# Kernel tuning notes

Hardware: AMD Instinct MI355X
Metric: run time of the kernel (lower is better)

The kernel has to match this reference:

```python
import jax, jax.numpy as jnp
import numpy as np
import math

N_HEAD, D_HEAD, D_MODEL = 12, 64, 768
ATT_SPAN = 512            # max_position_embeddings // stride**block_index
SCALE_FACTOR = 3          # 1 + 2 (relative attention: content + c2p + p2c)
CLS_TOKENS = 1            # num_highway_cls_tokens + 1
INF = 1e6
LN_EPS = 1e-5
SCALE = 1.0 / (math.sqrt(D_HEAD) * math.sqrt(SCALE_FACTOR))


def setup_inputs() -> dict:
    key = jax.random.key(0)
    ks = jax.random.split(key, 10)
    B, S = 2, 2048
    lin = lambda k, shape: jax.random.normal(k, shape, dtype=jnp.float32) * 0.02
    return {
        "query": jax.random.normal(ks[0], (B, S, D_MODEL), dtype=jnp.float32),
        "attention_mask": jnp.ones((B, S), dtype=jnp.float32),
        "pos_key_embed": jax.random.normal(ks[1], (2 * ATT_SPAN, D_MODEL), dtype=jnp.float32),
        "pos_query_embed": jax.random.normal(ks[2], (2 * ATT_SPAN, D_MODEL), dtype=jnp.float32),
        "Wq": lin(ks[3], (N_HEAD * D_HEAD, D_MODEL)),
        "bq": jnp.zeros((N_HEAD * D_HEAD,), dtype=jnp.float32),
        "Wk": lin(ks[4], (N_HEAD * D_HEAD, D_MODEL)),
        "Wv": lin(ks[5], (D_MODEL, D_MODEL)),
        "bv": jnp.zeros((D_MODEL,), dtype=jnp.float32),
        "Wpq": lin(ks[6], (N_HEAD * D_HEAD, D_MODEL)),
        "bpq": jnp.zeros((N_HEAD * D_HEAD,), dtype=jnp.float32),
        "Wpk": lin(ks[7], (N_HEAD * D_HEAD, D_MODEL)),
        "r_w_bias": jax.random.normal(ks[8], (N_HEAD, D_HEAD), dtype=jnp.float32) * 0.02,
        "ln_gamma": jnp.ones((D_MODEL,), dtype=jnp.float32),
        "ln_beta": jnp.zeros((D_MODEL,), dtype=jnp.float32),
    }


def _forward(query, attention_mask, pos_key_embed, pos_query_embed,
             Wq, bq, Wk, Wv, bv, Wpq, bpq, Wpk, r_w_bias, ln_gamma, ln_beta):
    B, S, _ = query.shape
    # self-attention: key = value = query
    v = query @ Wv.T + bv                                             # v_head projection
    qh = (query @ Wq.T + bq).reshape(B, S, N_HEAD, D_HEAD)
    kh = (query @ Wk.T).reshape(B, S, N_HEAD, D_HEAD)
    vh = v.reshape(B, S, N_HEAD, D_MODEL // N_HEAD)
    qh = (qh + r_w_bias) * SCALE                                       # bias + scale fused into q

    content = jnp.einsum('bind,bjnd->bnij', qh, kh)                    # [B,n,S,S]

    # ---- disentangled relative-position bias (DeBERTa-style c2p + p2c) ----
    pos_k = (pos_key_embed @ Wpk.T).reshape(2 * ATT_SPAN, N_HEAD, D_HEAD).transpose(1, 0, 2)          # [n,2span,d]
    pos_q = (pos_query_embed @ Wpq.T + bpq).reshape(2 * ATT_SPAN, N_HEAD, D_HEAD).transpose(1, 0, 2)  # [n,2span,d]
    qbn = qh.transpose(0, 2, 1, 3)                                     # [B,n,S,d] (already scaled)
    kbn = kh.transpose(0, 2, 1, 3)
    rel = jnp.arange(S)[:, None] - jnp.arange(S)[None, :]              # [S,S] query - key

    # content -> position
    c2p = jnp.einsum('bnid,njd->bnij', qbn, pos_k)                     # [B,n,S,2span]
    c2p_idx = jnp.clip(rel + ATT_SPAN, 0, 2 * ATT_SPAN - 1)
    c2p_score = jnp.take_along_axis(c2p, c2p_idx[None, None], axis=-1) # [B,n,S,S]

    # position -> content
    p2c = jnp.einsum('bnjd,nid->bnji', kbn * (1.0 / math.sqrt(D_HEAD * SCALE_FACTOR)), pos_q)  # [B,n,S,2span]
    p2c_idx = jnp.clip(-rel + ATT_SPAN, 0, 2 * ATT_SPAN - 1)
    p2c_score = jnp.take_along_axis(p2c, p2c_idx[None, None], axis=-1).swapaxes(-1, -2)        # [B,n,S,S]

    bias = c2p_score + p2c_score
    # zero out bias on cls rows and cls columns (the padding/concat trick in the source)
    keep = (jnp.arange(S) >= CLS_TOKENS).astype(bias.dtype)
    bias = bias * (keep[:, None] * keep[None, :])

    score = content + bias
    score = score - INF * (1.0 - attention_mask[:, None, None, :])
    prob = jax.nn.softmax(score, axis=-1)                              # attention_dropout = 0.0

    attn_vec = jnp.einsum('bnij,bjnd->bind', prob, vh).reshape(B, S, D_MODEL)
    # fused residual + LayerNorm(attn_out)
    mu = attn_vec.mean(-1, keepdims=True)
    var = ((attn_vec - mu) ** 2).mean(-1, keepdims=True)
    ln = (attn_vec - mu) / jnp.sqrt(var + LN_EPS) * ln_gamma + ln_beta
    return query + ln


def reference(query, attention_mask, pos_key_embed, pos_query_embed,
              Wq, bq, Wk, Wv, bv, Wpq, bpq, Wpk, r_w_bias, ln_gamma, ln_beta):
    return _forward(query, attention_mask, pos_key_embed, pos_query_embed,
                    Wq, bq, Wk, Wv, bv, Wpq, bpq, Wpk, r_w_bias, ln_gamma, ln_beta)
```

## Files before the change

### kernel.cpp

```cpp
#include <hip/hip_runtime.h>
#include <math.h>

#define NB     2
#define SEQ    2048
#define NHEAD  12
#define DMODEL 768
#define SPAN2  1024
#define SCALEF 0.07216878364870323f

typedef unsigned short ushort;
typedef unsigned int   uint;
typedef __attribute__((ext_vector_type(8))) short  bh8;
typedef __attribute__((ext_vector_type(4))) float  f32x4;
typedef __attribute__((ext_vector_type(4))) unsigned short us4;

__device__ inline ushort f2bf(float x) {
    uint u = __builtin_bit_cast(uint, x);
    u += 0x7FFFu + ((u >> 16) & 1u);
    return (ushort)(u >> 16);
}
__device__ inline float b2f(ushort h) {
    uint u = ((uint)h) << 16;
    return __builtin_bit_cast(float, u);
}

__device__ __forceinline__ void gld16(const ushort* g, ushort* l) {
    __builtin_amdgcn_global_load_lds(
        (const __attribute__((address_space(1))) void*)g,
        (__attribute__((address_space(3))) void*)l, 16, 0, 0);
}

__device__ __forceinline__ bh8 ldsfrag(const ushort* tile, int row, int slot) {
    return *(const bh8*)((const char*)tile + row * 128 + (((slot ^ (row & 7)) << 4)));
}

struct CvtArgs {
    const float* src[8];
    ushort*      dst[8];
    int          n[8];
};

__global__ __launch_bounds__(256) void cvt_bf16(CvtArgs a)
{
    const int seg = blockIdx.y;
    const int i   = (blockIdx.x * 256 + threadIdx.x) * 8;
    if (i >= a.n[seg]) return;
    const float4* s = (const float4*)(a.src[seg] + i);
    const float4 x = s[0], y = s[1];
    bh8 o;
    o[0] = (short)f2bf(x.x); o[1] = (short)f2bf(x.y);
    o[2] = (short)f2bf(x.z); o[3] = (short)f2bf(x.w);
    o[4] = (short)f2bf(y.x); o[5] = (short)f2bf(y.y);
    o[6] = (short)f2bf(y.z); o[7] = (short)f2bf(y.w);
    *(bh8*)(a.dst[seg] + i) = o;
}

__global__ __launch_bounds__(256) void proj_qkv(
    const ushort* __restrict__ X,
    const ushort* __restrict__ Wq, const ushort* __restrict__ Wk,
    const ushort* __restrict__ Wv,
    const float* __restrict__ bq, const float* __restrict__ rwb,
    const float* __restrict__ bv,
    ushort* __restrict__ qh, ushort* __restrict__ kh, ushort* __restrict__ vht)
{
    __shared__ ushort Xs [32 * 64];
    __shared__ ushort Wqs[64 * 64];
    __shared__ ushort Wks[64 * 64];
    __shared__ ushort Wvs[64 * 64];
    const int r0 = blockIdx.x * 32;
    const int n  = blockIdx.y;
    const int c0 = n * 64;
    const int tid  = threadIdx.x;
    const int w    = tid >> 6;
    const int lane = tid & 63;
    const int lo   = lane & 15;
    const int hi8  = (lane >> 4) * 8;
    const int g4   = (lane >> 4) * 4;
    const int wr   = w & 1;
    const int wc   = w >> 1;
    const int r8   = lane >> 3;
    const int sl   = lane & 7;
    const int slotA = hi8 >> 3;

    f32x4 aq[2] = {}, ak[2] = {}, av[2] = {};
    for (int k0 = 0; k0 < DMODEL; k0 += 64) {
        {
            const int r = w * 8 + r8;
            const int s = sl ^ (r & 7);
            gld16(X + (size_t)(r0 + r) * DMODEL + k0 + s * 8, Xs + w * 512);
        }
        #pragma unroll
        for (int i = 0; i < 2; ++i) {
            const int c = i * 4 + w;
            const int r = c * 8 + r8;
            const int s = sl ^ (r & 7);
            gld16(Wq + (size_t)(c0 + r) * DMODEL + k0 + s * 8, Wqs + c * 512);
            gld16(Wk + (size_t)(c0 + r) * DMODEL + k0 + s * 8, Wks + c * 512);
            gld16(Wv + (size_t)(c0 + r) * DMODEL + k0 + s * 8, Wvs + c * 512);
        }
        __syncthreads();
        const bh8 a0 = ldsfrag(Xs, wr * 16 + lo, slotA);
        const bh8 a1 = ldsfrag(Xs, wr * 16 + lo, 4 + slotA);
        #pragma unroll
        for (int ct = 0; ct < 2; ++ct) {
            const int row = wc * 32 + ct * 16 + lo;
            aq[ct] = __builtin_amdgcn_mfma_f32_16x16x32_bf16(a0, ldsfrag(Wqs, row, slotA),     aq[ct], 0, 0, 0);
            aq[ct] = __builtin_amdgcn_mfma_f32_16x16x32_bf16(a1, ldsfrag(Wqs, row, 4 + slotA), aq[ct], 0, 0, 0);
            ak[ct] = __builtin_amdgcn_mfma_f32_16x16x32_bf16(a0, ldsfrag(Wks, row, slotA),     ak[ct], 0, 0, 0);
            ak[ct] = __builtin_amdgcn_mfma_f32_16x16x32_bf16(a1, ldsfrag(Wks, row, 4 + slotA), ak[ct], 0, 0, 0);
            av[ct] = __builtin_amdgcn_mfma_f32_16x16x32_bf16(a0, ldsfrag(Wvs, row, slotA),     av[ct], 0, 0, 0);
            av[ct] = __builtin_amdgcn_mfma_f32_16x16x32_bf16(a1, ldsfrag(Wvs, row, 4 + slotA), av[ct], 0, 0, 0);
        }
        __syncthreads();
    }

    const int rbase = r0 + wr * 16 + g4;
    const int bb  = rbase >> 11;
    const int rr0 = rbase & (SEQ - 1);
    #pragma unroll
    for (int ct = 0; ct < 2; ++ct) {
        const int d = wc * 32 + ct * 16 + lo;
        const int c = c0 + d;
        const float bqv = bq[c] + rwb[c];
        const float bvv = bv[c];
        us4 o;
        #pragma unroll
        for (int reg = 0; reg < 4; ++reg) {
            const size_t rowi = ((size_t)bb * NHEAD + n) * SEQ + rr0 + reg;
            qh[rowi * 64 + d] = f2bf((aq[ct][reg] + bqv) * SCALEF);
            kh[rowi * 64 + d] = f2bf(ak[ct][reg]);
            o[reg] = f2bf(av[ct][reg] + bvv);
        }
        *(us4*)&vht[(((size_t)bb * NHEAD + n) * 64 + d) * SEQ + rr0] = o;
    }
}

__global__ __launch_bounds__(256) void proj_pos(
    const ushort* __restrict__ PKe, const ushort* __restrict__ PQe,
    const ushort* __restrict__ Wpk, const ushort* __restrict__ Wpq,
    const float* __restrict__ bpq,
    ushort* __restrict__ pkp, ushort* __restrict__ pqp)
{
    __shared__ ushort Xk [32 * 64];
    __shared__ ushort Xq [32 * 64];
    __shared__ ushort Wks[64 * 64];
    __shared__ ushort Wqs[64 * 64];
    const int r0 = blockIdx.x * 32;
    const int n  = blockIdx.y;
    const int c0 = n * 64;
    const int tid  = threadIdx.x;
    const int w    = tid >> 6;
    const int lane = tid & 63;
    const int lo   = lane & 15;
    const int hi8  = (lane >> 4) * 8;
    const int g4   = (lane >> 4) * 4;
    const int wr   = w & 1;
    const int wc   = w >> 1;
    const int r8   = lane >> 3;
    const int sl   = lane & 7;
    const int slotA = hi8 >> 3;

    f32x4 apk[2] = {}, apq[2] = {};
    for (int k0 = 0; k0 < DMODEL; k0 += 64) {
        {
            const int r = w * 8 + r8;
            const int s = sl ^ (r & 7);
            gld16(PKe + (size_t)(r0 + r) * DMODEL + k0 + s * 8, Xk + w * 512);
            gld16(PQe + (size_t)(r0 + r) * DMODEL + k0 + s * 8, Xq + w * 512);
        }
        #pragma unroll
        for (int i = 0; i < 2; ++i) {
            const int c = i * 4 + w;
            const int r = c * 8 + r8;
            const int s = sl ^ (r & 7);
            gld16(Wpk + (size_t)(c0 + r) * DMODEL + k0 + s * 8, Wks + c * 512);
            gld16(Wpq + (size_t)(c0 + r) * DMODEL + k0 + s * 8, Wqs + c * 512);
        }
        __syncthreads();
        const bh8 xk0 = ldsfrag(Xk, wr * 16 + lo, slotA);
        const bh8 xk1 = ldsfrag(Xk, wr * 16 + lo, 4 + slotA);
        const bh8 xq0 = ldsfrag(Xq, wr * 16 + lo, slotA);
        const bh8 xq1 = ldsfrag(Xq, wr * 16 + lo, 4 + slotA);
        #pragma unroll
        for (int ct = 0; ct < 2; ++ct) {
            const int row = wc * 32 + ct * 16 + lo;
            apk[ct] = __builtin_amdgcn_mfma_f32_16x16x32_bf16(xk0, ldsfrag(Wks, row, slotA),     apk[ct], 0, 0, 0);
            apk[ct] = __builtin_amdgcn_mfma_f32_16x16x32_bf16(xk1, ldsfrag(Wks, row, 4 + slotA), apk[ct], 0, 0, 0);
            apq[ct] = __builtin_amdgcn_mfma_f32_16x16x32_bf16(xq0, ldsfrag(Wqs, row, slotA),     apq[ct], 0, 0, 0);
            apq[ct] = __builtin_amdgcn_mfma_f32_16x16x32_bf16(xq1, ldsfrag(Wqs, row, 4 + slotA), apq[ct], 0, 0, 0);
        }
        __syncthreads();
    }

    const int rr0 = r0 + wr * 16 + g4;
    #pragma unroll
    for (int ct = 0; ct < 2; ++ct) {
        const int d = wc * 32 + ct * 16 + lo;
        const int c = c0 + d;
        const float badd = bpq[c];
        #pragma unroll
        for (int reg = 0; reg < 4; ++reg) {
            const size_t rowi = ((size_t)n * SPAN2 + rr0 + reg);
            pkp[rowi * 64 + d] = f2bf(apk[ct][reg]);
            pqp[rowi * 64 + d] = f2bf((apq[ct][reg] + badd) * SCALEF);
        }
    }
}

__global__ __launch_bounds__(256) void cd_vec(
    const ushort* __restrict__ qh, const ushort* __restrict__ kh,
    const ushort* __restrict__ posk, const ushort* __restrict__ posq,
    float* __restrict__ cdv)
{
    __shared__ float pr[4][64];
    const int bn = blockIdx.y;
    const int n  = bn % NHEAD;
    const int tid = threadIdx.x;
    if (tid < 64) {
        pr[0][tid] = b2f(posk[((size_t)n * SPAN2) * 64 + tid]);
        pr[1][tid] = b2f(posk[((size_t)n * SPAN2 + SPAN2 - 1) * 64 + tid]);
        pr[2][tid] = b2f(posq[((size_t)n * SPAN2) * 64 + tid]);
        pr[3][tid] = b2f(posq[((size_t)n * SPAN2 + SPAN2 - 1) * 64 + tid]);
    }
    __syncthreads();
    const int row = blockIdx.x * 32 + (tid >> 3);
    const int e0  = (tid & 7) * 8;
    const bh8 q8 = *(const bh8*)&qh[((size_t)bn * SEQ + row) * 64 + e0];
    const bh8 k8 = *(const bh8*)&kh[((size_t)bn * SEQ + row) * 64 + e0];
    float a0 = 0.f, a1 = 0.f, a2 = 0.f, a3 = 0.f;
    #pragma unroll
    for (int t = 0; t < 8; ++t) {
        const float qv = b2f((ushort)q8[t]);
        const float kv = b2f((ushort)k8[t]);
        a0 += qv * pr[0][e0 + t];
        a1 += qv * pr[1][e0 + t];
        a2 += kv * pr[2][e0 + t];
        a3 += kv * pr[3][e0 + t];
    }
    #pragma unroll
    for (int off = 1; off <= 4; off <<= 1) {
        a0 += __shfl_xor(a0, off);
        a1 += __shfl_xor(a1, off);
        a2 += __shfl_xor(a2, off);
        a3 += __shfl_xor(a3, off);
    }
    if ((tid & 7) == 0) {
        cdv[((size_t)0 * NB * NHEAD + bn) * SEQ + row] = a0;
        cdv[((size_t)1 * NB * NHEAD + bn) * SEQ + row] = a1;
        cdv[((size_t)2 * NB * NHEAD + bn) * SEQ + row] = a2;
        cdv[((size_t)3 * NB * NHEAD + bn) * SEQ + row] = a3;
    }
}

__global__ __launch_bounds__(256, 3) void attn_mfma10(
    const ushort* __restrict__ qh, const ushort* __restrict__ kh,
    const ushort* __restrict__ vht, const ushort* __restrict__ posk,
    const ushort* __restrict__ posq, const float* __restrict__ mask,
    const float* __restrict__ cdv, float* __restrict__ attn)
{
    __shared__ ushort POS[128 * 64];
    __shared__ ushort Kb [64 * 64];
    __shared__ ushort Vb [64 * 64];
    __shared__ ushort T1c[64 * 68];
    __shared__ ushort T2c[64 * 68];

    const int id   = blockIdx.x;
    const int xcd  = id & 7;
    const int slot = id >> 3;
    const int bn   = xcd * 3 + (slot >> 5);
    const int i0   = (slot & 31) * 64;
    const int b    = bn / NHEAD;
    const int n    = bn % NHEAD;

    const int tid  = threadIdx.x;
    const int w    = tid >> 6;
    const int lane = tid & 63;
    const int lo   = lane & 15;
    const int hi8  = (lane >> 4) * 8;
    const int g4   = (lane >> 4) * 4;
    const int w16  = w * 16;
    const int r8   = lane >> 3;
    const int sl   = lane & 7;
    const int slotA = hi8 >> 3;

    const ushort* qrow = qh + ((size_t)bn * SEQ + i0 + w16 + lo) * 64;
    const bh8 qa0 = *(const bh8*)&qrow[hi8];
    const bh8 qa1 = *(const bh8*)&qrow[32 + hi8];

    const ushort* khb = kh   + (size_t)bn * SEQ * 64;
    const ushort* vtb = vht  + (size_t)bn * 64 * SEQ;
    const ushort* pkh = posk + (size_t)n * SPAN2 * 64;
    const ushort* pqh = posq + (size_t)n * SPAN2 * 64;
    const float*  mrw = mask + (size_t)b * SEQ;

    float C0r[4], C1r[4];
    {
        const float* C0p = cdv + (size_t)bn * SEQ;
        const float* C1p = cdv + ((size_t)NB * NHEAD + bn) * SEQ;
        #pragma unroll
        for (int reg = 0; reg < 4; ++reg) {
            C0r[reg] = C0p[i0 + w16 + g4 + reg];
            C1r[reg] = C1p[i0 + w16 + g4 + reg];
        }
    }
    const float* D0p = cdv + ((size_t)2 * NB * NHEAD + bn) * SEQ;
    const float* D1p = cdv + ((size_t)3 * NB * NHEAD + bn) * SEQ;

    f32x4 accPV[4] = {};
    float mrow[4] = {-1e30f, -1e30f, -1e30f, -1e30f};
    float lrow[4] = {0.f, 0.f, 0.f, 0.f};

    for (int j0 = 0; j0 < SEQ; j0 += 64) {
        const int d0base = i0 - j0 + 449;
        const bool clamp0 = (d0base <= -126);
        const bool clamp1 = (d0base >= 1023);

        if (!clamp0 && !clamp1) {
        #pragma unroll
        for (int i = 0; i < 2; ++i) {
            const int c = i * 4 + w;
            const int r = c * 8 + r8;
            const int s = sl ^ (r & 7);
            gld16(khb + (size_t)(j0 + r) * 64 + s * 8, Kb + c * 512);
        }
        #pragma unroll
        for (int i = 0; i < 4; ++i) {
            const int c = i * 4 + w;
            const int r = c * 8 + r8;
            const int s = sl ^ (r & 7);
            int gr = d0base + r; gr = gr < 0 ? 0 : (gr > SPAN2 - 1 ? SPAN2 - 1 : gr);
            gld16(pkh + (size_t)gr * 64 + s * 8, POS + c * 512);
        }
        __syncthreads();

        const bh8 ka0 = ldsfrag(Kb, w16 + lo, slotA);
        const bh8 ka1 = ldsfrag(Kb, w16 + lo, 4 + slotA);
        f32x4 z1[5];
        #pragma unroll
        for (int q = 0; q < 5; ++q) {
            const int u1 = (w + q) * 16 + lo;
            const bh8 pk0 = ldsfrag(POS, u1, slotA);
            const bh8 pk1 = ldsfrag(POS, u1, 4 + slotA);
            f32x4 a = {};
            a = __builtin_amdgcn_mfma_f32_16x16x32_bf16(qa0, pk0, a, 0, 0, 0);
            z1[q] = __builtin_amdgcn_mfma_f32_16x16x32_bf16(qa1, pk1, a, 0, 0, 0);
        }
        __syncthreads();

        #pragma unroll
        for (int i = 0; i < 4; ++i) {
            const int c = i * 4 + w;
            const int r = c * 8 + r8;
            const int s = sl ^ (r & 7);
            int gr = d0base + r; gr = gr < 0 ? 0 : (gr > SPAN2 - 1 ? SPAN2 - 1 : gr);
            gld16(pqh + (size_t)gr * 64 + s * 8, POS + c * 512);
        }
        #pragma unroll
        for (int i = 0; i < 2; ++i) {
            const int c = i * 4 + w;
            const int r = c * 8 + r8;
            const int s = sl ^ (r & 7);
            gld16(vtb + (size_t)r * SEQ + j0 + s * 8, Vb + c * 512);
        }
        #pragma unroll
        for (int q = 0; q < 5; ++q)
            #pragma unroll
            for (int reg = 0; reg < 4; ++reg) {
                const int cc2 = q * 16 + lo - g4 - reg;
                if (cc2 >= 0 && cc2 < 64)
                    T1c[(w16 + g4 + reg) * 68 + cc2] = f2bf(z1[q][reg]);
            }
        f32x4 accS[4];
        #pragma unroll
        for (int ct = 0; ct < 4; ++ct) {
            const bh8 kb0 = ldsfrag(Kb, ct * 16 + lo, slotA);
            const bh8 kb1 = ldsfrag(Kb, ct * 16 + lo, 4 + slotA);
            f32x4 z = {};
            z = __builtin_amdgcn_mfma_f32_16x16x32_bf16(qa0, kb0, z, 0, 0, 0);
            accS[ct] = __builtin_amdgcn_mfma_f32_16x16x32_bf16(qa1, kb1, z, 0, 0, 0);
        }
        float maskadd[4];
        #pragma unroll
        for (int ct = 0; ct < 4; ++ct)
            maskadd[ct] = -1e6f * (1.f - mrw[j0 + ct * 16 + lo]);
        __syncthreads();

        #pragma unroll
        for (int q = 0; q < 5; ++q) {
            const int u2 = (3 - w + q) * 16 + lo;
            const bh8 pq0 = ldsfrag(POS, u2, slotA);
            const bh8 pq1 = ldsfrag(POS, u2, 4 + slotA);
            f32x4 z = {};
            z = __builtin_amdgcn_mfma_f32_16x16x32_bf16(ka0, pq0, z, 0, 0, 0);
            z = __builtin_amdgcn_mfma_f32_16x16x32_bf16(ka1, pq1, z, 0, 0, 0);
            #pragma unroll
            for (int reg = 0; reg < 4; ++reg) {
                const int il2 = q * 16 + lo + g4 + reg - 15;
                if (il2 >= 0 && il2 < 64)
                    T2c[(w16 + g4 + reg) * 68 + il2] = f2bf(z[reg]);
            }
        }
        __syncthreads();

        float corr[4];
        char* pbase = (char*)POS + w * 2048;
        #pragma unroll
        for (int reg = 0; reg < 4; ++reg) {
            const int il = w16 + g4 + reg;
            const int gi = i0 + il;
            float s[4], rmax = -1e30f;
            #pragma unroll
            for (int ct = 0; ct < 4; ++ct) {
                const int jl = ct * 16 + lo;
                float v = accS[ct][reg];
                if (gi >= 1 && (j0 + jl) >= 1)
                    v += b2f(T1c[il * 68 + 63 - jl]) + b2f(T2c[jl * 68 + il]);
                v += maskadd[ct];
                s[ct] = v;
                rmax = fmaxf(rmax, v);
            }
            rmax = fmaxf(rmax, __shfl_xor(rmax, 1));
            rmax = fmaxf(rmax, __shfl_xor(rmax, 2));
            rmax = fmaxf(rmax, __shfl_xor(rmax, 4));
            rmax = fmaxf(rmax, __shfl_xor(rmax, 8));
            const float mnew = fmaxf(mrow[reg], rmax);
            const float cc   = __expf(mrow[reg] - mnew);
            float psum = 0.f;
            const int prow = g4 + reg;
            #pragma unroll
            for (int ct = 0; ct < 4; ++ct) {
                const float p = __expf(s[ct] - mnew);
                psum += p;
                *(ushort*)(pbase + prow * 128 + ((((ct * 16 + lo) * 2)) ^ ((prow & 7) * 16))) = f2bf(p);
            }
            psum += __shfl_xor(psum, 1);
            psum += __shfl_xor(psum, 2);
            psum += __shfl_xor(psum, 4);
            psum += __shfl_xor(psum, 8);
            lrow[reg] = lrow[reg] * cc + psum;
            mrow[reg] = mnew;
            corr[reg] = cc;
        }

        {
            const bh8 pa0 = *(const bh8*)(pbase + lo * 128 + ((slotA << 4) ^ ((lo & 7) * 16)));
            const bh8 pa1 = *(const bh8*)(pbase + lo * 128 + (((4 + slotA) << 4) ^ ((lo & 7) * 16)));
            #pragma unroll
            for (int dt = 0; dt < 4; ++dt) {
                const bh8 vb0 = ldsfrag(Vb, dt * 16 + lo, slotA);
                const bh8 vb1 = ldsfrag(Vb, dt * 16 + lo, 4 + slotA);
                f32x4 a = accPV[dt];
                #pragma unroll
                for (int reg = 0; reg < 4; ++reg) a[reg] *= corr[reg];
                a = __builtin_amdgcn_mfma_f32_16x16x32_bf16(pa0, vb0, a, 0, 0, 0);
                accPV[dt] = __builtin_amdgcn_mfma_f32_16x16x32_bf16(pa1, vb1, a, 0, 0, 0);
            }
        }
        __syncthreads();

        } else {
        const float* Dp = clamp0 ? D0p : D1p;
        float Dvv[4];
        #pragma unroll
        for (int ct = 0; ct < 4; ++ct)
            Dvv[ct] = Dp[j0 + ct * 16 + lo];
        float maskadd[4];
        #pragma unroll
        for (int ct = 0; ct < 4; ++ct)
            maskadd[ct] = -1e6f * (1.f - mrw[j0 + ct * 16 + lo]);

        #pragma unroll
        for (int i = 0; i < 2; ++i) {
            const int c = i * 4 + w;
            const int r = c * 8 + r8;
            const int s = sl ^ (r & 7);
            gld16(khb + (size_t)(j0 + r) * 64 + s * 8, Kb + c * 512);
            gld16(vtb + (size_t)r * SEQ + j0 + s * 8, Vb + c * 512);
        }
        __syncthreads();

        f32x4 accS[4];
        #pragma unroll
        for (int ct = 0; ct < 4; ++ct) {
            const bh8 kb0 = ldsfrag(Kb, ct * 16 + lo, slotA);
            const bh8 kb1 = ldsfrag(Kb, ct * 16 + lo, 4 + slotA);
            f32x4 z = {};
            z = __builtin_amdgcn_mfma_f32_16x16x32_bf16(qa0, kb0, z, 0, 0, 0);
            accS[ct] = __builtin_amdgcn_mfma_f32_16x16x32_bf16(qa1, kb1, z, 0, 0, 0);
        }

        float corr[4];
        char* pbase = (char*)POS + w * 2048;
        #pragma unroll
        for (int reg = 0; reg < 4; ++reg) {
            const int il = w16 + g4 + reg;
            const int gi = i0 + il;
            const float Cvv = clamp0 ? C0r[reg] : C1r[reg];
            float s[4], rmax = -1e30f;
            #pragma unroll
            for (int ct = 0; ct < 4; ++ct) {
                const int jl = ct * 16 + lo;
                float v = accS[ct][reg];
                if (gi >= 1 && (j0 + jl) >= 1)
                    v += Cvv + Dvv[ct];
                v += maskadd[ct];
                s[ct] = v;
                rmax = fmaxf(rmax, v);
            }
            rmax = fmaxf(rmax, __shfl_xor(rmax, 1));
            rmax = fmaxf(rmax, __shfl_xor(rmax, 2));
            rmax = fmaxf(rmax, __shfl_xor(rmax, 4));
            rmax = fmaxf(rmax, __shfl_xor(rmax, 8));
            const float mnew = fmaxf(mrow[reg], rmax);
            const float cc   = __expf(mrow[reg] - mnew);
            float psum = 0.f;
            const int prow = g4 + reg;
            #pragma unroll
            for (int ct = 0; ct < 4; ++ct) {
                const float p = __expf(s[ct] - mnew);
                psum += p;
                *(ushort*)(pbase + prow * 128 + ((((ct * 16 + lo) * 2)) ^ ((prow & 7) * 16))) = f2bf(p);
            }
            psum += __shfl_xor(psum, 1);
            psum += __shfl_xor(psum, 2);
            psum += __shfl_xor(psum, 4);
            psum += __shfl_xor(psum, 8);
            lrow[reg] = lrow[reg] * cc + psum;
            mrow[reg] = mnew;
            corr[reg] = cc;
        }

        {
            const bh8 pa0 = *(const bh8*)(pbase + lo * 128 + ((slotA << 4) ^ ((lo & 7) * 16)));
            const bh8 pa1 = *(const bh8*)(pbase + lo * 128 + (((4 + slotA) << 4) ^ ((lo & 7) * 16)));
            #pragma unroll
            for (int dt = 0; dt < 4; ++dt) {
                const bh8 vb0 = ldsfrag(Vb, dt * 16 + lo, slotA);
                const bh8 vb1 = ldsfrag(Vb, dt * 16 + lo, 4 + slotA);
                f32x4 a = accPV[dt];
                #pragma unroll
                for (int reg = 0; reg < 4; ++reg) a[reg] *= corr[reg];
                a = __builtin_amdgcn_mfma_f32_16x16x32_bf16(pa0, vb0, a, 0, 0, 0);
                accPV[dt] = __builtin_amdgcn_mfma_f32_16x16x32_bf16(pa1, vb1, a, 0, 0, 0);
            }
        }
        __syncthreads();
        }
    }

    #pragma unroll
    for (int reg = 0; reg < 4; ++reg) {
        const int i = i0 + w16 + g4 + reg;
        const float inv = 1.f / lrow[reg];
        #pragma unroll
        for (int dt = 0; dt < 4; ++dt)
            attn[((size_t)b * SEQ + i) * DMODEL + n * 64 + dt * 16 + lo] =
                accPV[dt][reg] * inv;
    }
}

__global__ __launch_bounds__(256) void resid_ln(
    float* __restrict__ attn, const float* __restrict__ query,
    const float* __restrict__ gamma, const float* __restrict__ beta)
{
    const int b = blockIdx.y;
    const int i = blockIdx.x;
    const size_t base = ((size_t)b * SEQ + i) * DMODEL;
    const int tid = threadIdx.x;

    float x[3];
    #pragma unroll
    for (int s = 0; s < 3; ++s) x[s] = attn[base + s * 256 + tid];

    float sum = x[0] + x[1] + x[2];
    float sq  = x[0]*x[0] + x[1]*x[1] + x[2]*x[2];
    #pragma unroll
    for (int off = 32; off; off >>= 1) {
        sum += __shfl_xor(sum, off);
        sq  += __shfl_xor(sq, off);
    }
    __shared__ float red[2][4];
    const int w = tid >> 6;
    if ((tid & 63) == 0) { red[0][w] = sum; red[1][w] = sq; }
    __syncthreads();
    sum = red[0][0] + red[0][1] + red[0][2] + red[0][3];
    sq  = red[1][0] + red[1][1] + red[1][2] + red[1][3];

    const float mu  = sum * (1.f / DMODEL);
    const float var = sq * (1.f / DMODEL) - mu * mu;
    const float inv = rsqrtf(var + 1e-5f);

    #pragma unroll
    for (int s = 0; s < 3; ++s) {
        const int c = s * 256 + tid;
        attn[base + c] = query[base + c] + (x[s] - mu) * inv * gamma[c] + beta[c];
    }
}

extern "C" void kernel_launch(void* const* d_in, const int* in_sizes, int n_in,
                              void* d_out, int out_size, void* d_ws, size_t ws_size,
                              hipStream_t stream)
{
    const float* query = (const float*)d_in[0];
    const float* mask  = (const float*)d_in[1];
    const float* pke   = (const float*)d_in[2];
    const float* pqe   = (const float*)d_in[3];
    const float* Wq    = (const float*)d_in[4];
    const float* bq    = (const float*)d_in[5];
    const float* Wk    = (const float*)d_in[6];
    const float* Wv    = (const float*)d_in[7];
    const float* bv    = (const float*)d_in[8];
    const float* Wpq   = (const float*)d_in[9];
    const float* bpq   = (const float*)d_in[10];
    const float* Wpk   = (const float*)d_in[11];
    const float* rwb   = (const float*)d_in[12];
    const float* gamma = (const float*)d_in[13];
    const float* beta  = (const float*)d_in[14];

    float* out = (float*)d_out;

    const int Q_N  = NB * SEQ * DMODEL;
    const int P_N  = SPAN2 * DMODEL;
    const int W_N  = DMODEL * DMODEL;
    const size_t QKV_ELEMS = (size_t)NB * NHEAD * SEQ * 64;
    const size_t POS_ELEMS = (size_t)NHEAD * SPAN2 * 64;

    ushort* xb   = (ushort*)d_ws;
    ushort* pkeb = xb   + Q_N;
    ushort* pqeb = pkeb + P_N;
    ushort* wqb  = pqeb + P_N;
    ushort* wkb  = wqb  + W_N;
    ushort* wvb  = wkb  + W_N;
    ushort* wpqb = wvb  + W_N;
    ushort* wpkb = wpqb + W_N;
    ushort* qh   = wpkb + W_N;
    ushort* kh   = qh   + QKV_ELEMS;
    ushort* vht  = kh   + QKV_ELEMS;
    ushort* pkp  = vht  + QKV_ELEMS;
    ushort* pqp  = pkp  + POS_ELEMS;
    float*  cdv  = (float*)(pqp + POS_ELEMS);

    dim3 blk(256);

    CvtArgs ca;
    ca.src[0] = query; ca.dst[0] = xb;   ca.n[0] = Q_N;
    ca.src[1] = pke;   ca.dst[1] = pkeb; ca.n[1] = P_N;
    ca.src[2] = pqe;   ca.dst[2] = pqeb; ca.n[2] = P_N;
    ca.src[3] = Wq;    ca.dst[3] = wqb;  ca.n[3] = W_N;
    ca.src[4] = Wk;    ca.dst[4] = wkb;  ca.n[4] = W_N;
    ca.src[5] = Wv;    ca.dst[5] = wvb;  ca.n[5] = W_N;
    ca.src[6] = Wpq;   ca.dst[6] = wpqb; ca.n[6] = W_N;
    ca.src[7] = Wpk;   ca.dst[7] = wpkb; ca.n[7] = W_N;
    cvt_bf16<<<dim3((Q_N / 8 + 255) / 256, 8), blk, 0, stream>>>(ca);

    proj_qkv<<<dim3(NB * SEQ / 32, NHEAD), blk, 0, stream>>>(
        xb, wqb, wkb, wvb, bq, rwb, bv, qh, kh, vht);
    proj_pos<<<dim3(SPAN2 / 32, NHEAD), blk, 0, stream>>>(
        pkeb, pqeb, wpkb, wpqb, bpq, pkp, pqp);

    cd_vec<<<dim3(SEQ / 32, NB * NHEAD), blk, 0, stream>>>(
        qh, kh, pkp, pqp, cdv);

    attn_mfma10<<<dim3(NB * NHEAD * (SEQ / 64)), blk, 0, stream>>>(
        qh, kh, vht, pkp, pqp, mask, cdv, out);

    resid_ln<<<dim3(SEQ, NB), blk, 0, stream>>>(out, query, gamma, beta);
}
```

Measured before the change: 213.4 us.

## Enlarge QKV projection row tile and transpose relative-bias staging buffers

The QKV projection now gives each block 64 rows instead of 32, so every weight tile loaded into shared memory is reused across twice as many rows and each wave computes four column tiles. In the attention kernel, both relative-position bias tiles are written transposed into shared memory. The CLS masking and the key mask are applied at write time, so the softmax stage can read four contiguous bias values per column with vector loads and no per-element branching. This trades fewer projection blocks and more accumulator registers for lower shared-memory read cost in the attention inner loop.

```diff
diff --git a/kernel.cpp b/kernel.cpp
--- a/kernel.cpp
+++ b/kernel.cpp
@@ -63,11 +63,11 @@
     const float* __restrict__ bv,
     ushort* __restrict__ qh, ushort* __restrict__ kh, ushort* __restrict__ vht)
 {
-    __shared__ ushort Xs [32 * 64];
+    __shared__ ushort Xs [64 * 64];
     __shared__ ushort Wqs[64 * 64];
     __shared__ ushort Wks[64 * 64];
     __shared__ ushort Wvs[64 * 64];
-    const int r0 = blockIdx.x * 32;
+    const int r0 = blockIdx.x * 64;
     const int n  = blockIdx.y;
     const int c0 = n * 64;
     const int tid  = threadIdx.x;
@@ -76,34 +76,29 @@
     const int lo   = lane & 15;
     const int hi8  = (lane >> 4) * 8;
     const int g4   = (lane >> 4) * 4;
-    const int wr   = w & 1;
-    const int wc   = w >> 1;
+    const int w16  = w * 16;
     const int r8   = lane >> 3;
     const int sl   = lane & 7;
     const int slotA = hi8 >> 3;
 
-    f32x4 aq[2] = {}, ak[2] = {}, av[2] = {};
+    f32x4 aq[4] = {}, ak[4] = {}, av[4] = {};
     for (int k0 = 0; k0 < DMODEL; k0 += 64) {
-        {
-            const int r = w * 8 + r8;
-            const int s = sl ^ (r & 7);
-            gld16(X + (size_t)(r0 + r) * DMODEL + k0 + s * 8, Xs + w * 512);
-        }
         #pragma unroll
         for (int i = 0; i < 2; ++i) {
             const int c = i * 4 + w;
             const int r = c * 8 + r8;
             const int s = sl ^ (r & 7);
+            gld16(X  + (size_t)(r0 + r) * DMODEL + k0 + s * 8, Xs  + c * 512);
             gld16(Wq + (size_t)(c0 + r) * DMODEL + k0 + s * 8, Wqs + c * 512);
             gld16(Wk + (size_t)(c0 + r) * DMODEL + k0 + s * 8, Wks + c * 512);
             gld16(Wv + (size_t)(c0 + r) * DMODEL + k0 + s * 8, Wvs + c * 512);
         }
         __syncthreads();
-        const bh8 a0 = ldsfrag(Xs, wr * 16 + lo, slotA);
-        const bh8 a1 = ldsfrag(Xs, wr * 16 + lo, 4 + slotA);
-        #pragma unroll
-        for (int ct = 0; ct < 2; ++ct) {
-            const int row = wc * 32 + ct * 16 + lo;
+        const bh8 a0 = ldsfrag(Xs, w16 + lo, slotA);
+        const bh8 a1 = ldsfrag(Xs, w16 + lo, 4 + slotA);
+        #pragma unroll
+        for (int ct = 0; ct < 4; ++ct) {
+            const int row = ct * 16 + lo;
             aq[ct] = __builtin_amdgcn_mfma_f32_16x16x32_bf16(a0, ldsfrag(Wqs, row, slotA),     aq[ct], 0, 0, 0);
             aq[ct] = __builtin_amdgcn_mfma_f32_16x16x32_bf16(a1, ldsfrag(Wqs, row, 4 + slotA), aq[ct], 0, 0, 0);
             ak[ct] = __builtin_amdgcn_mfma_f32_16x16x32_bf16(a0, ldsfrag(Wks, row, slotA),     ak[ct], 0, 0, 0);
@@ -114,12 +109,12 @@
         __syncthreads();
     }
 
-    const int rbase = r0 + wr * 16 + g4;
+    const int rbase = r0 + w16 + g4;
     const int bb  = rbase >> 11;
     const int rr0 = rbase & (SEQ - 1);
     #pragma unroll
-    for (int ct = 0; ct < 2; ++ct) {
-        const int d = wc * 32 + ct * 16 + lo;
+    for (int ct = 0; ct < 4; ++ct) {
+        const int d = ct * 16 + lo;
         const int c = c0 + d;
         const float bqv = bq[c] + rwb[c];
         const float bvv = bv[c];
@@ -252,7 +247,7 @@
     }
 }
 
-__global__ __launch_bounds__(256, 3) void attn_mfma10(
+__global__ __launch_bounds__(256, 3) void attn_mfma11(
     const ushort* __restrict__ qh, const ushort* __restrict__ kh,
     const ushort* __restrict__ vht, const ushort* __restrict__ posk,
     const ushort* __restrict__ posq, const float* __restrict__ mask,
@@ -261,8 +256,8 @@
     __shared__ ushort POS[128 * 64];
     __shared__ ushort Kb [64 * 64];
     __shared__ ushort Vb [64 * 64];
-    __shared__ ushort T1c[64 * 68];
-    __shared__ ushort T2c[64 * 68];
+    __shared__ ushort TB1[64 * 68];
+    __shared__ ushort TB2[64 * 68];
 
     const int id   = blockIdx.x;
     const int xcd  = id & 7;
@@ -366,9 +361,12 @@
         for (int q = 0; q < 5; ++q)
             #pragma unroll
             for (int reg = 0; reg < 4; ++reg) {
-                const int cc2 = q * 16 + lo - g4 - reg;
-                if (cc2 >= 0 && cc2 < 64)
-                    T1c[(w16 + g4 + reg) * 68 + cc2] = f2bf(z1[q][reg]);
+                const int jl = g4 + reg - q * 16 - lo + 63;
+                if (jl >= 0 && jl < 64) {
+                    const int il = w16 + g4 + reg;
+                    const float v = ((i0 + il) >= 1 && (j0 + jl) >= 1) ? z1[q][reg] : 0.f;
+                    TB1[jl * 68 + il] = f2bf(v);
+                }
             }
         f32x4 accS[4];
         #pragma unroll
@@ -379,10 +377,10 @@
             z = __builtin_amdgcn_mfma_f32_16x16x32_bf16(qa0, kb0, z, 0, 0, 0);
             accS[ct] = __builtin_amdgcn_mfma_f32_16x16x32_bf16(qa1, kb1, z, 0, 0, 0);
         }
-        float maskadd[4];
-        #pragma unroll
-        for (int ct = 0; ct < 4; ++ct)
-            maskadd[ct] = -1e6f * (1.f - mrw[j0 + ct * 16 + lo]);
+        float madd[4];
+        #pragma unroll
+        for (int reg = 0; reg < 4; ++reg)
+            madd[reg] = -1e6f * (1.f - mrw[j0 + w16 + g4 + reg]);
         __syncthreads();
 
         #pragma unroll
@@ -395,30 +393,31 @@
             z = __builtin_amdgcn_mfma_f32_16x16x32_bf16(ka1, pq1, z, 0, 0, 0);
             #pragma unroll
             for (int reg = 0; reg < 4; ++reg) {
-                const int il2 = q * 16 + lo + g4 + reg - 15;
-                if (il2 >= 0 && il2 < 64)
-                    T2c[(w16 + g4 + reg) * 68 + il2] = f2bf(z[reg]);
+                const int il = (3 + q) * 16 + lo + g4 + reg - 63;
+                if (il >= 0 && il < 64) {
+                    const int jl = w16 + g4 + reg;
+                    const float v = ((i0 + il) >= 1 && (j0 + jl) >= 1) ? z[reg] : 0.f;
+                    TB2[jl * 68 + il] = f2bf(v + madd[reg]);
+                }
             }
         }
         __syncthreads();
 
+        float sv[4][4];
+        #pragma unroll
+        for (int ct = 0; ct < 4; ++ct) {
+            const int jl = ct * 16 + lo;
+            const us4 t1 = *(const us4*)&TB1[jl * 68 + w16 + g4];
+            const us4 t2 = *(const us4*)&TB2[jl * 68 + w16 + g4];
+            #pragma unroll
+            for (int reg = 0; reg < 4; ++reg)
+                sv[reg][ct] = accS[ct][reg] + b2f(t1[reg]) + b2f(t2[reg]);
+        }
         float corr[4];
         char* pbase = (char*)POS + w * 2048;
         #pragma unroll
         for (int reg = 0; reg < 4; ++reg) {
-            const int il = w16 + g4 + reg;
-            const int gi = i0 + il;
-            float s[4], rmax = -1e30f;
-            #pragma unroll
-            for (int ct = 0; ct < 4; ++ct) {
-                const int jl = ct * 16 + lo;
-                float v = accS[ct][reg];
-                if (gi >= 1 && (j0 + jl) >= 1)
-                    v += b2f(T1c[il * 68 + 63 - jl]) + b2f(T2c[jl * 68 + il]);
-                v += maskadd[ct];
-                s[ct] = v;
-                rmax = fmaxf(rmax, v);
-            }
+            float rmax = fmaxf(fmaxf(sv[reg][0], sv[reg][1]), fmaxf(sv[reg][2], sv[reg][3]));
             rmax = fmaxf(rmax, __shfl_xor(rmax, 1));
             rmax = fmaxf(rmax, __shfl_xor(rmax, 2));
             rmax = fmaxf(rmax, __shfl_xor(rmax, 4));
@@ -429,7 +428,7 @@
             const int prow = g4 + reg;
             #pragma unroll
             for (int ct = 0; ct < 4; ++ct) {
-                const float p = __expf(s[ct] - mnew);
+                const float p = __expf(sv[reg][ct] - mnew);
                 psum += p;
                 *(ushort*)(pbase + prow * 128 + ((((ct * 16 + lo) * 2)) ^ ((prow & 7) * 16))) = f2bf(p);
             }
@@ -653,7 +652,7 @@
     ca.src[7] = Wpk;   ca.dst[7] = wpkb; ca.n[7] = W_N;
     cvt_bf16<<<dim3((Q_N / 8 + 255) / 256, 8), blk, 0, stream>>>(ca);
 
-    proj_qkv<<<dim3(NB * SEQ / 32, NHEAD), blk, 0, stream>>>(
+    proj_qkv<<<dim3(NB * SEQ / 64, NHEAD), blk, 0, stream>>>(
         xb, wqb, wkb, wvb, bq, rwb, bv, qh, kh, vht);
     proj_pos<<<dim3(SPAN2 / 32, NHEAD), blk, 0, stream>>>(
         pkeb, pqeb, wpkb, wpqb, bpq, pkp, pqp);
@@ -661,7 +660,7 @@
     cd_vec<<<dim3(SEQ / 32, NB * NHEAD), blk, 0, stream>>>(
         qh, kh, pkp, pqp, cdv);
 
-    attn_mfma10<<<dim3(NB * NHEAD * (SEQ / 64)), blk, 0, stream>>>(
+    attn_mfma11<<<dim3(NB * NHEAD * (SEQ / 64)), blk, 0, stream>>>(
         qh, kh, vht, pkp, pqp, mask, cdv, out);
 
     resid_ln<<<dim3(SEQ, NB), blk, 0, stream>>>(out, query, gamma, beta);
```

Measured after the change: 211.6 us. About the same (-0.9%).
